# Performance work log

Measured on AMD Instinct MI355X. Metric: run time of the kernel, lower is better.

## Reference

```python
import jax, jax.numpy as jnp
import numpy as np

J = 25
C_IN, HID, LAT = 3, 64, 32


def _graph_conv(x, A, W, b):
    # x: [N,T,J,Cin]; A: [J,J]; W: [Cin,Cout]; b: [Cout]
    A = jax.nn.softmax(A, axis=-1)
    # fused adjacency mix + projection: (A @ x) @ W + b
    x = jnp.einsum('ij,ntjc->ntic', A, x)
    return jnp.einsum('ntjc,cd->ntjd', x, W) + b


def setup_inputs() -> dict:
    key = jax.random.key(0)
    ks = jax.random.split(key, 13)
    x = jax.random.normal(ks[0], (32, 2048, J, C_IN), dtype=jnp.float32)
    eye = jnp.eye(J, dtype=jnp.float32)
    def lin(kw, kb, cin, cout):
        W = jax.random.normal(kw, (cin, cout), dtype=jnp.float32) / np.sqrt(cin)
        b = jax.random.normal(kb, (cout,), dtype=jnp.float32) * 0.01
        return W, b
    W1, b1 = lin(ks[1], ks[2], C_IN, HID)
    W2, b2 = lin(ks[3], ks[4], HID, LAT)
    W3, b3 = lin(ks[5], ks[6], LAT, HID)
    W4, b4 = lin(ks[7], ks[8], HID, C_IN)
    return {
        'x': x,
        'A1': eye, 'W1': W1, 'b1': b1,
        'A2': eye, 'W2': W2, 'b2': b2,
        'A3': eye, 'W3': W3, 'b3': b3,
        'A4': eye, 'W4': W4, 'b4': b4,
    }


def reference(x, A1, W1, b1, A2, W2, b2, A3, W3, b3, A4, W4, b4):
    h = jax.nn.relu(_graph_conv(x, A1, W1, b1))     # encoder_g1 + relu
    z = _graph_conv(h, A2, W2, b2)                  # encoder_g2 (no relu)
    h_dec = jax.nn.relu(_graph_conv(z, A3, W3, b3)) # decoder_g1 + relu
    out = _graph_conv(h_dec, A4, W4, b4)            # decoder_g2
    return out
```

## Files before the change

kernel.cpp:

```cpp
#include <hip/hip_runtime.h>
#include <math.h>

#define J 25
#define NJC 75
#define NWAVE 4
#define NTHREADS 256
#define NFPW 16

#define O_A1P  0
#define O_APP  1024
#define O_A4B  2048
#define O_W2T  3072
#define O_W3T  5120
#define O_W1A  7168
#define O_W4C  8192
#define O_B4   8512
#define O_BPPF 8576
#define CWS_SZ 8704

using bf16x2 = __attribute__((ext_vector_type(2))) __bf16;
using bf16x8 = __attribute__((ext_vector_type(8))) __bf16;
using f32x4  = __attribute__((ext_vector_type(4))) float;
using f32x16 = __attribute__((ext_vector_type(16))) float;

__device__ inline bf16x8 zero8() {
    bf16x8 z;
    #pragma unroll
    for (int j = 0; j < 8; j++) z[j] = (__bf16)0.f;
    return z;
}

#if defined(__has_builtin)
#if __has_builtin(__builtin_amdgcn_cvt_pk_bf16_f32)
#define HAVE_PK_BF16 1
#endif
#endif

__device__ inline bf16x2 cvt2(float a, float b) {
#ifdef HAVE_PK_BF16
    return __builtin_amdgcn_cvt_pk_bf16_f32(a, b);
#else
    bf16x2 r; r[0] = (__bf16)a; r[1] = (__bf16)b; return r;
#endif
}
__device__ inline bf16x8 pk8(const f32x16& acc, int st) {
    const int b = 8 * st;
    bf16x8 r;
    #pragma unroll
    for (int p = 0; p < 4; p++) {
        bf16x2 v = cvt2(acc[b + 2 * p], acc[b + 2 * p + 1]);
        r[2 * p] = v[0]; r[2 * p + 1] = v[1];
    }
    return r;
}

__global__ __launch_bounds__(NTHREADS, 2) void gcn_fused(
    const float* __restrict__ x,
    const float* __restrict__ A1, const float* __restrict__ W1, const float* __restrict__ b1,
    const float* __restrict__ A2, const float* __restrict__ W2, const float* __restrict__ b2,
    const float* __restrict__ A3, const float* __restrict__ W3, const float* __restrict__ b3,
    const float* __restrict__ A4, const float* __restrict__ W4, const float* __restrict__ b4,
    float* __restrict__ out)
{
    __shared__ __align__(16) float  TS[3189];
    __shared__ __align__(16) __bf16 CWS[CWS_SZ];

    const int t = threadIdx.x;

    {
        float* T   = TS;
        float* bpp = T + 3125;
        float* T0 = T;        float* T1 = T + 625;  float* T2 = T + 1250;
        float* T3 = T + 1875; float* T4 = T + 2500;

        if (t < 100) {
            const int m = t / J, i = t % J;
            const float* Asrc = (m == 0) ? A1 : (m == 1) ? A2 : (m == 2) ? A3 : A4;
            float row[J];
            float mx = -1e30f;
            #pragma unroll
            for (int j = 0; j < J; j++) { row[j] = Asrc[i * J + j]; mx = fmaxf(mx, row[j]); }
            float s = 0.f;
            #pragma unroll
            for (int j = 0; j < J; j++) { row[j] = __expf(row[j] - mx); s += row[j]; }
            const float inv = 1.f / s;
            float* dst = T + m * 625 + i * J;
            #pragma unroll
            for (int j = 0; j < J; j++) dst[j] = row[j] * inv;
        }
        if (t < 64) {
            float s = b3[t];
            #pragma unroll
            for (int l = 0; l < 32; l++) s += W3[l * 64 + t] * b2[l];
            bpp[t] = s;
        }
        __syncthreads();

        for (int idx = t; idx < 625; idx += 256) {
            const int i = idx / J, jj = idx % J;
            float s = 0.f;
            #pragma unroll
            for (int k = 0; k < J; k++) s += T2[i * J + k] * T1[k * J + jj];
            T4[idx] = s;
        }
        __syncthreads();

        for (int i = t; i < 1024; i += 256) {
            const int b = i >> 8, n = (i >> 3) & 31, jj = i & 7;
            const int s = b >> 1, h = b & 1, r = 8 * s + jj;
            const int k32 = (r & 3) + 8 * (r >> 2) + 4 * h;
            const bool ok = (k32 < J && n < J);
            CWS[O_A1P + i] = (__bf16)(ok ? T0[n * J + k32] : 0.f);
            CWS[O_APP + i] = (__bf16)(ok ? T4[n * J + k32] : 0.f);
            CWS[O_A4B + i] = (__bf16)(ok ? T3[n * J + k32] : 0.f);
        }
        for (int i = t; i < 2048; i += 256) {
            {
                const int b = i >> 8, n = (i >> 3) & 31, jj = i & 7;
                const int s = b >> 1, h = b & 1, r = 8 * (s & 1) + jj;
                const int d = 32 * (s >> 1) + (r & 3) + 8 * (r >> 2) + 4 * h;
                CWS[O_W2T + i] = (__bf16)W2[d * 32 + n];
            }
            {
                const int tt = i >> 10, rr = i & 1023;
                const int b = rr >> 8, m = (rr >> 3) & 31, jj = rr & 7;
                const int s = b >> 1, h = b & 1, r = 8 * s + jj;
                const int l = (r & 3) + 8 * (r >> 2) + 4 * h;
                CWS[O_W3T + i] = (__bf16)W3[l * 64 + tt * 32 + m];
            }
        }
        for (int i = t; i < 1024; i += 256) {
            const int tile = i >> 9, rr = i & 511, hf_ = rr >> 8, n = (rr >> 3) & 31, jj = rr & 7;
            const int k = 8 * hf_ + jj;
            const int d = tile * 32 + n;
            float v = 0.f;
            if (k < 3) v = W1[k * 64 + d];
            else if (k == 3) v = b1[d];
            CWS[O_W1A + i] = (__bf16)v;
        }
        {
            const int c = t >> 6, b = (t >> 3) & 7, jj = t & 7;
            const int s = b >> 1, h = b & 1, r = 8 * (s & 1) + jj;
            const int d = 32 * (s >> 1) + (r & 3) + 8 * (r >> 2) + 4 * h;
            CWS[O_W4C + t] = (c < 3) ? (__bf16)W4[d * 3 + c] : (__bf16)0.f;
        }
        {
            float* fwB = (float*)(CWS + O_BPPF);
            if (t < 64) {
                const int g = t >> 4, h = (t >> 3) & 1, jj = t & 7;
                const int tt = g >> 1, st = g & 1;
                const int row32 = (jj & 3) + 16 * st + 8 * (jj >> 2) + 4 * h;
                fwB[t] = bpp[tt * 32 + row32];
            }
            float* fb4 = (float*)(CWS + O_B4);
            if (t >= 64 && t < 68) fb4[t - 64] = (t < 67) ? b4[t - 64] : 0.f;
        }
        __syncthreads();
    }

    const int w = t >> 6, lane = t & 63, ln = lane & 31, half = lane >> 5;
    const int fo = ln * 8;

    const long fbase = ((long)blockIdx.x * NWAVE + w) * NFPW;

    const float* xp = x + fbase * NJC;
    float* op = out + fbase * NJC;

    const bool xact = (lane < J);
    const int xoff = lane * 3;

    float xA0 = 0.f, xA1 = 0.f, xA2 = 0.f;
    float xB0 = 0.f, xB1 = 0.f, xB2 = 0.f;
    if (xact) {
        const float* q = xp + xoff;
        xA0 = q[0]; xA1 = q[1]; xA2 = q[2];
    }
    xp += NJC;
    if (xact) {
        const float* q = xp + xoff;
        xB0 = q[0]; xB1 = q[1]; xB2 = q[2];
    }
    xp += NJC;

    bf16x8 rA1P[2], rApp[2], rA4b[2], rW1A[2], rW2[4], rW3[4], rW4[4];
    #pragma unroll
    for (int ks = 0; ks < 2; ks++) {
        rA1P[ks] = *(const bf16x8*)&CWS[O_A1P + (2 * ks + half) * 256 + fo];
        rApp[ks] = *(const bf16x8*)&CWS[O_APP + (2 * ks + half) * 256 + fo];
        rA4b[ks] = *(const bf16x8*)&CWS[O_A4B + (2 * ks + half) * 256 + fo];
        rW1A[ks] = *(const bf16x8*)&CWS[O_W1A + ks * 512 + half * 256 + fo];
    }
    #pragma unroll
    for (int ks = 0; ks < 4; ks++)
        rW2[ks] = *(const bf16x8*)&CWS[O_W2T + (half + 2 * ks) * 256 + fo];
    #pragma unroll
    for (int tt = 0; tt < 2; tt++)
        #pragma unroll
        for (int ks = 0; ks < 2; ks++)
            rW3[tt * 2 + ks] = *(const bf16x8*)&CWS[O_W3T + tt * 1024 + (half + 2 * ks) * 256 + fo];
    #pragma unroll
    for (int ks = 0; ks < 4; ks++) {
        rW4[ks] = zero8();
        if (ln < 3) rW4[ks] = *(const bf16x8*)&CWS[O_W4C + ln * 64 + (half + 2 * ks) * 8];
    }
    f32x16 rB16[2];
    {
        const float* fwB = (const float*)(CWS + O_BPPF);
        #pragma unroll
        for (int tt = 0; tt < 2; tt++)
            #pragma unroll
            for (int st = 0; st < 2; st++) {
                f32x4 qa = *(const f32x4*)&fwB[32 * tt + 16 * st + 8 * half + 0];
                f32x4 qb = *(const f32x4*)&fwB[32 * tt + 16 * st + 8 * half + 4];
                #pragma unroll
                for (int j = 0; j < 4; j++) {
                    rB16[tt][8 * st + j]     = qa[j];
                    rB16[tt][8 * st + 4 + j] = qb[j];
                }
            }
    }
    const float* fb4 = (const float*)(CWS + O_B4);
    const float b40 = fb4[0], b41 = fb4[1], b42 = fb4[2];

    f32x16 Z;
    #pragma unroll
    for (int z = 0; z < 16; z++) Z[z] = 0.f;

    const bool do_store = (lane < J);

    auto frame = [&](bf16x8 xa, float* opp) {
        f32x16 accG0 = __builtin_amdgcn_mfma_f32_32x32x16_bf16(xa, rW1A[0], Z, 0, 0, 0);
        f32x16 accG1 = __builtin_amdgcn_mfma_f32_32x32x16_bf16(xa, rW1A[1], Z, 0, 0, 0);
        bf16x8 ga0 = pk8(accG0, 0), ga1 = pk8(accG0, 1);
        bf16x8 ga2 = pk8(accG1, 0), ga3 = pk8(accG1, 1);

        bf16x8 hf[4];
        {
            f32x16 accH0 = __builtin_amdgcn_mfma_f32_32x32x16_bf16(ga0, rA1P[0], Z, 0, 0, 0);
            accH0 = __builtin_amdgcn_mfma_f32_32x32x16_bf16(ga1, rA1P[1], accH0, 0, 0, 0);
            f32x16 accH1 = __builtin_amdgcn_mfma_f32_32x32x16_bf16(ga2, rA1P[0], Z, 0, 0, 0);
            accH1 = __builtin_amdgcn_mfma_f32_32x32x16_bf16(ga3, rA1P[1], accH1, 0, 0, 0);
            #pragma unroll
            for (int z = 0; z < 16; z++) {
                accH0[z] = fmaxf(accH0[z], 0.f);
                accH1[z] = fmaxf(accH1[z], 0.f);
            }
            hf[0] = pk8(accH0, 0); hf[1] = pk8(accH0, 1);
            hf[2] = pk8(accH1, 0); hf[3] = pk8(accH1, 1);
        }

        f32x16 accU = __builtin_amdgcn_mfma_f32_32x32x16_bf16(hf[0], rW2[0], Z, 0, 0, 0);
        #pragma unroll
        for (int s = 1; s < 4; s++)
            accU = __builtin_amdgcn_mfma_f32_32x32x16_bf16(hf[s], rW2[s], accU, 0, 0, 0);
        bf16x8 uf[2] = { pk8(accU, 0), pk8(accU, 1) };

        f32x16 accV = __builtin_amdgcn_mfma_f32_32x32x16_bf16(uf[0], rApp[0], Z, 0, 0, 0);
        accV = __builtin_amdgcn_mfma_f32_32x32x16_bf16(uf[1], rApp[1], accV, 0, 0, 0);
        bf16x8 vf[2] = { pk8(accV, 0), pk8(accV, 1) };

        bf16x8 hd[4];
        #pragma unroll
        for (int tt = 0; tt < 2; tt++) {
            f32x16 acc = __builtin_amdgcn_mfma_f32_32x32x16_bf16(rW3[tt * 2 + 0], vf[0], rB16[tt], 0, 0, 0);
            acc = __builtin_amdgcn_mfma_f32_32x32x16_bf16(rW3[tt * 2 + 1], vf[1], acc, 0, 0, 0);
            #pragma unroll
            for (int z = 0; z < 16; z++) acc[z] = fmaxf(acc[z], 0.f);
            hd[2 * tt]     = pk8(acc, 0);
            hd[2 * tt + 1] = pk8(acc, 1);
        }

        f32x16 accP = __builtin_amdgcn_mfma_f32_32x32x16_bf16(hd[0], rW4[0], Z, 0, 0, 0);
        #pragma unroll
        for (int s = 1; s < 4; s++)
            accP = __builtin_amdgcn_mfma_f32_32x32x16_bf16(hd[s], rW4[s], accP, 0, 0, 0);
        bf16x8 pf[2] = { pk8(accP, 0), pk8(accP, 1) };

        f32x16 accO = __builtin_amdgcn_mfma_f32_32x32x16_bf16(pf[0], rA4b[0], Z, 0, 0, 0);
        accO = __builtin_amdgcn_mfma_f32_32x32x16_bf16(pf[1], rA4b[1], accO, 0, 0, 0);
        if (do_store) {
            opp[lane * 3 + 0] = accO[0] + b40;
            opp[lane * 3 + 1] = accO[1] + b41;
            opp[lane * 3 + 2] = accO[2] + b42;
        }
    };

    #pragma unroll 1
    for (int fi = 0; fi < NFPW; fi += 2) {
        bf16x8 xaA = zero8();
        if (xact) {
            xaA[0] = (__bf16)xA0; xaA[1] = (__bf16)xA1;
            xaA[2] = (__bf16)xA2; xaA[3] = (__bf16)1.f;
        }
        if (fi + 2 < NFPW) {
            if (xact) {
                const float* q = xp + xoff;
                xA0 = q[0]; xA1 = q[1]; xA2 = q[2];
            }
        }
        xp += NJC;
        frame(xaA, op);
        op += NJC;

        bf16x8 xaB = zero8();
        if (xact) {
            xaB[0] = (__bf16)xB0; xaB[1] = (__bf16)xB1;
            xaB[2] = (__bf16)xB2; xaB[3] = (__bf16)1.f;
        }
        if (fi + 3 < NFPW) {
            if (xact) {
                const float* q = xp + xoff;
                xB0 = q[0]; xB1 = q[1]; xB2 = q[2];
            }
        }
        xp += NJC;
        frame(xaB, op);
        op += NJC;
    }
}

extern "C" void kernel_launch(void* const* d_in, const int* in_sizes, int n_in,
                              void* d_out, int out_size, void* d_ws, size_t ws_size,
                              hipStream_t stream)
{
    const float* x  = (const float*)d_in[0];
    const float* A1 = (const float*)d_in[1];
    const float* W1 = (const float*)d_in[2];
    const float* b1 = (const float*)d_in[3];
    const float* A2 = (const float*)d_in[4];
    const float* W2 = (const float*)d_in[5];
    const float* b2 = (const float*)d_in[6];
    const float* A3 = (const float*)d_in[7];
    const float* W3 = (const float*)d_in[8];
    const float* b3 = (const float*)d_in[9];
    const float* A4 = (const float*)d_in[10];
    const float* W4 = (const float*)d_in[11];
    const float* b4 = (const float*)d_in[12];
    float* out = (float*)d_out;
    (void)d_ws; (void)ws_size;

    const int NT = in_sizes[0] / NJC;
    const int nblocks = NT / (NWAVE * NFPW);

    gcn_fused<<<nblocks, NTHREADS, 0, stream>>>(
        x, A1, W1, b1, A2, W2, b2, A3, W3, b3, A4, W4, b4, out);
}
```

Baseline: 141.8 us.

## Raise occupancy by reloading bias per frame and halving frames per wave

Moves the decoder bias accumulators out of persistent registers and reloads them from LDS inside each frame, which cuts register pressure so launch bounds can ask for 3 blocks per SM instead of 2. Frames per wave is halved, so more blocks are launched. The two decoder MFMA chains are interleaved to expose independent work. In exchange, every frame pays extra LDS reads, and if the register budget is not met the compiler may spill.

```diff
diff --git a/kernel.cpp b/kernel.cpp
--- a/kernel.cpp
+++ b/kernel.cpp
@@ -5,7 +5,7 @@
 #define NJC 75
 #define NWAVE 4
 #define NTHREADS 256
-#define NFPW 16
+#define NFPW 8
 
 #define O_A1P  0
 #define O_APP  1024
@@ -54,7 +54,7 @@
     return r;
 }
 
-__global__ __launch_bounds__(NTHREADS, 2) void gcn_fused(
+__global__ __launch_bounds__(NTHREADS, 3) void gcn_fused(
     const float* __restrict__ x,
     const float* __restrict__ A1, const float* __restrict__ W1, const float* __restrict__ b1,
     const float* __restrict__ A2, const float* __restrict__ W2, const float* __restrict__ b2,
@@ -203,22 +203,8 @@
         rW4[ks] = zero8();
         if (ln < 3) rW4[ks] = *(const bf16x8*)&CWS[O_W4C + ln * 64 + (half + 2 * ks) * 8];
     }
-    f32x16 rB16[2];
-    {
-        const float* fwB = (const float*)(CWS + O_BPPF);
-        #pragma unroll
-        for (int tt = 0; tt < 2; tt++)
-            #pragma unroll
-            for (int st = 0; st < 2; st++) {
-                f32x4 qa = *(const f32x4*)&fwB[32 * tt + 16 * st + 8 * half + 0];
-                f32x4 qb = *(const f32x4*)&fwB[32 * tt + 16 * st + 8 * half + 4];
-                #pragma unroll
-                for (int j = 0; j < 4; j++) {
-                    rB16[tt][8 * st + j]     = qa[j];
-                    rB16[tt][8 * st + 4 + j] = qb[j];
-                }
-            }
-    }
+    const float* fwB = (const float*)(CWS + O_BPPF);
+
     const float* fb4 = (const float*)(CWS + O_B4);
     const float b40 = fb4[0], b41 = fb4[1], b42 = fb4[2];
 
@@ -255,19 +241,39 @@
             accU = __builtin_amdgcn_mfma_f32_32x32x16_bf16(hf[s], rW2[s], accU, 0, 0, 0);
         bf16x8 uf[2] = { pk8(accU, 0), pk8(accU, 1) };
 
+        f32x16 rb0, rb1;
+        #pragma unroll
+        for (int st = 0; st < 2; st++) {
+            f32x4 qa0 = *(const f32x4*)&fwB[16 * st + 8 * half + 0];
+            f32x4 qb0 = *(const f32x4*)&fwB[16 * st + 8 * half + 4];
+            f32x4 qa1 = *(const f32x4*)&fwB[32 + 16 * st + 8 * half + 0];
+            f32x4 qb1 = *(const f32x4*)&fwB[32 + 16 * st + 8 * half + 4];
+            #pragma unroll
+            for (int j = 0; j < 4; j++) {
+                rb0[8 * st + j]     = qa0[j];
+                rb0[8 * st + 4 + j] = qb0[j];
+                rb1[8 * st + j]     = qa1[j];
+                rb1[8 * st + 4 + j] = qb1[j];
+            }
+        }
+
         f32x16 accV = __builtin_amdgcn_mfma_f32_32x32x16_bf16(uf[0], rApp[0], Z, 0, 0, 0);
         accV = __builtin_amdgcn_mfma_f32_32x32x16_bf16(uf[1], rApp[1], accV, 0, 0, 0);
         bf16x8 vf[2] = { pk8(accV, 0), pk8(accV, 1) };
 
         bf16x8 hd[4];
-        #pragma unroll
-        for (int tt = 0; tt < 2; tt++) {
-            f32x16 acc = __builtin_amdgcn_mfma_f32_32x32x16_bf16(rW3[tt * 2 + 0], vf[0], rB16[tt], 0, 0, 0);
-            acc = __builtin_amdgcn_mfma_f32_32x32x16_bf16(rW3[tt * 2 + 1], vf[1], acc, 0, 0, 0);
-            #pragma unroll
-            for (int z = 0; z < 16; z++) acc[z] = fmaxf(acc[z], 0.f);
-            hd[2 * tt]     = pk8(acc, 0);
-            hd[2 * tt + 1] = pk8(acc, 1);
+        {
+            f32x16 acc0 = __builtin_amdgcn_mfma_f32_32x32x16_bf16(rW3[0], vf[0], rb0, 0, 0, 0);
+            acc0 = __builtin_amdgcn_mfma_f32_32x32x16_bf16(rW3[1], vf[1], acc0, 0, 0, 0);
+            f32x16 acc1 = __builtin_amdgcn_mfma_f32_32x32x16_bf16(rW3[2], vf[0], rb1, 0, 0, 0);
+            acc1 = __builtin_amdgcn_mfma_f32_32x32x16_bf16(rW3[3], vf[1], acc1, 0, 0, 0);
+            #pragma unroll
+            for (int z = 0; z < 16; z++) {
+                acc0[z] = fmaxf(acc0[z], 0.f);
+                acc1[z] = fmaxf(acc1[z], 0.f);
+            }
+            hd[0] = pk8(acc0, 0); hd[1] = pk8(acc0, 1);
+            hd[2] = pk8(acc1, 0); hd[3] = pk8(acc1, 1);
         }
 
         f32x16 accP = __builtin_amdgcn_mfma_f32_32x32x16_bf16(hd[0], rW4[0], Z, 0, 0, 0);
```

Result: slower. 151.6 us (+7.0%).
